# Kernel tuning notes

Measured on AMD Instinct MI355X. Metric: run time of the kernel, lower is better.

## Reference

```python
import jax, jax.numpy as jnp
import numpy as np

B, S, C, D = 16, 8192, 32, 3
VEC_OUT = 16
OUT_CH = 128
NEG_SLOPE = 0.2
EPS = float(np.finfo(np.float64).eps)


def setup_inputs() -> dict:
    key = jax.random.key(0)
    k1, k2, k3, k4, k5 = jax.random.split(key, 5)
    x = jax.random.normal(k1, (B, S, C, D), dtype=jnp.float32)
    x = x / jnp.linalg.norm(x, axis=-1, keepdims=True)  # project onto S^2
    n_in = C - 1  # 31
    U0 = (jax.random.truncated_normal(k2, -2.0, 2.0, (VEC_OUT, n_in)) * np.sqrt(2.0 / n_in)).astype(jnp.float32)
    W0 = (jax.random.truncated_normal(k3, -2.0, 2.0, (VEC_OUT, n_in)) / np.sqrt(n_in) + 1.0 / n_in).astype(jnp.float32)
    feat = n_in * VEC_OUT  # 496
    dense_kernel = (jax.random.normal(k4, (feat, OUT_CH)) / np.sqrt(feat)).astype(jnp.float32)
    dense_bias = jnp.zeros((OUT_CH,), dtype=jnp.float32)
    return {"x": x, "U0": U0, "W0": W0, "dense_kernel": dense_kernel, "dense_bias": dense_bias}


def _sphere_log(p, q):
    # p: [N, D] base points, q: [N, C-1, D]; log_p(q) on unit sphere
    cos = jnp.clip(jnp.sum(p[:, None, :] * q, axis=-1), -1.0, 1.0)  # [N, C-1]
    theta = jnp.arccos(cos)
    sin_safe = jnp.where(theta < 1e-6, 1.0, jnp.sin(theta))
    fac = jnp.where(theta < 1e-6, 1.0, theta / sin_safe)
    return fac[..., None] * (q - cos[..., None] * p[:, None, :])  # [N, C-1, D]


def _vn_layer(w, U, W):
    # w: [B, S, n_in, D]
    k = jnp.einsum('ij,bsjd->bsid', U, w)
    q = jnp.einsum('ij,bsjd->bsid', W, w)
    sqnrm_k = jnp.sum(k * k, axis=-1, keepdims=True) + EPS
    dot_qk = jnp.sum(q * k, axis=-1, keepdims=True)
    h = q + k * jax.nn.relu(-dot_qk) / sqnrm_k
    return NEG_SLOPE * q + (1.0 - NEG_SLOPE) * h


def reference(x, U0, W0, dense_kernel, dense_bias):
    n_batch, n_seq, n_in = x.shape[:3]
    xf = x.reshape(-1, n_in, D)            # [N, C, D]
    p = xf[:, 0]                           # base points
    v = _sphere_log(p, xf[:, 1:])          # [N, C-1, D]
    w = v.reshape(n_batch, n_seq, n_in - 1, D)
    w = _vn_layer(w, U0, W0)               # [B, S, VEC_OUT, D]
    w = w.reshape(n_batch * n_seq, VEC_OUT, D)
    # metric.flat on the sphere (induced metric) is the identity; VEC_OUT <= n_in so flat applies to w
    y = jnp.einsum('nij,nkj->nik', v, w)   # [N, C-1, VEC_OUT]
    y = y.reshape(n_batch, n_seq, -1)
    return y @ dense_kernel + dense_bias   # [B, S, OUT_CH]
```

## Files before the change

kernel.cpp:

```cpp
#include <hip/hip_runtime.h>

typedef float float4v __attribute__((ext_vector_type(4)));
typedef short short8  __attribute__((ext_vector_type(8)));

#define TOKENS_PER_BLOCK 256
#define NBLOCKS 512

__device__ __forceinline__ short f2bf(float f) {
  unsigned u = __float_as_uint(f);
  unsigned r = (u + 0x7fffu + ((u >> 16) & 1u)) >> 16;
  return (short)r;
}

__global__ __launch_bounds__(256, 2)
void tangent_fused(const float* __restrict__ x,
                   const float* __restrict__ U0,
                   const float* __restrict__ W0,
                   const float* __restrict__ dk,
                   const float* __restrict__ bias,
                   float* __restrict__ out)
{
  __shared__ __align__(16) float xlds[16 * 100];
  __shared__ __align__(16) float vlds[16 * 104];
  __shared__ __align__(16) float u0p[16 * 36];
  __shared__ __align__(16) float w0p[16 * 36];
  __shared__ __align__(16) short ylds[16 * 520];

  const int tid  = threadIdx.x;
  const int lane = tid & 63;
  const int wv   = tid >> 6;

  for (int i = tid; i < 16 * 36; i += 256) { u0p[i] = 0.f; w0p[i] = 0.f; }
  __syncthreads();
  for (int i = tid; i < 496; i += 256) {
    int r = i / 31, c = i % 31;
    u0p[r * 36 + c] = U0[i];
    w0p[r * 36 + c] = W0[i];
  }

  const int bn  = lane & 15;
  const int k8  = (lane >> 4) * 8;
  const int ch0 = wv * 32;
  short8 bfrag[16][2];
#pragma unroll
  for (int kk = 0; kk < 16; ++kk) {
#pragma unroll
    for (int g = 0; g < 2; ++g) {
      int c = ch0 + 16 * g + bn;
      short8 t;
#pragma unroll
      for (int j = 0; j < 8; ++j) {
        int f = kk * 32 + k8 + j;
        float v = (f < 496) ? dk[f * 128 + c] : 0.f;
        t[j] = f2bf(v);
      }
      bfrag[kk][g] = t;
    }
  }
  const float bias0 = bias[ch0 + bn];
  const float bias1 = bias[ch0 + 16 + bn];
  __syncthreads();

  const int tok16 = tid >> 4;
  const int tt    = tid & 15;

  const int block_tok0 = blockIdx.x * TOKENS_PER_BLOCK;

  for (int tile = 0; tile < 16; ++tile) {
    const int tbase = block_tok0 + tile * 16;

    {
      const float4v* xg = (const float4v*)(x + (size_t)tbase * 96);
      {
        int idx = tid;
        float4v v = xg[idx];
        int tk = idx / 24, cl = (idx % 24) * 4;
        *(float4v*)&xlds[tk * 100 + cl] = v;
      }
      {
        int idx = tid + 256;
        if (idx < 384) {
          float4v v = xg[idx];
          int tk = idx / 24, cl = (idx % 24) * 4;
          *(float4v*)&xlds[tk * 100 + cl] = v;
        }
      }
    }
    __syncthreads();

    {
      const float* xr = &xlds[tok16 * 100];
      float p0 = xr[0], p1 = xr[1], p2 = xr[2];
      float* vr = &vlds[tok16 * 104];
#pragma unroll
      for (int rep = 0; rep < 2; ++rep) {
        int jj = tt + rep * 16;
        if (jj < 31) {
          float q0 = xr[3 + 3 * jj], q1 = xr[4 + 3 * jj], q2 = xr[5 + 3 * jj];
          float cs = __fadd_rn(__fadd_rn(__fmul_rn(p0, q0), __fmul_rn(p1, q1)),
                               __fmul_rn(p2, q2));
          cs = fminf(fmaxf(cs, -1.f), 1.f);
          float th  = acosf(cs);
          float fac = (th < 1e-6f) ? 1.f : (th / sinf(th));
          vr[3 * jj + 0] = fac * (q0 - cs * p0);
          vr[3 * jj + 1] = fac * (q1 - cs * p1);
          vr[3 * jj + 2] = fac * (q2 - cs * p2);
        }
      }
      if (tt == 15) { vr[93] = 0.f; vr[94] = 0.f; vr[95] = 0.f; }
    }
    __syncthreads();

    {
      const float4v* v4 = (const float4v*)&vlds[tok16 * 104];
      const float4v* u4 = (const float4v*)&u0p[tt * 36];
      const float4v* w4 = (const float4v*)&w0p[tt * 36];
      float k0 = 0, k1 = 0, k2 = 0, q0 = 0, q1 = 0, q2 = 0;
#pragma unroll
      for (int g = 0; g < 8; ++g) {
        float4v a = v4[3 * g], b = v4[3 * g + 1], c = v4[3 * g + 2];
        float4v uu = u4[g], ww = w4[g];
        k0 += uu.x * a.x; k1 += uu.x * a.y; k2 += uu.x * a.z;
        q0 += ww.x * a.x; q1 += ww.x * a.y; q2 += ww.x * a.z;
        k0 += uu.y * a.w; k1 += uu.y * b.x; k2 += uu.y * b.y;
        q0 += ww.y * a.w; q1 += ww.y * b.x; q2 += ww.y * b.y;
        k0 += uu.z * b.z; k1 += uu.z * b.w; k2 += uu.z * c.x;
        q0 += ww.z * b.z; q1 += ww.z * b.w; q2 += ww.z * c.x;
        k0 += uu.w * c.y; k1 += uu.w * c.z; k2 += uu.w * c.w;
        q0 += ww.w * c.y; q1 += ww.w * c.z; q2 += ww.w * c.w;
      }
      float dot = k0 * q0 + k1 * q1 + k2 * q2;
      float sq  = k0 * k0 + k1 * k1 + k2 * k2 + 2.2204460492503131e-16f;
      float fac = fmaxf(-dot, 0.f) / sq;
      float f8  = 0.8f * fac;
      float wx = q0 + f8 * k0, wy = q1 + f8 * k1, wz = q2 + f8 * k2;

      asm volatile("" ::: "memory");

      short* yrow = &ylds[tok16 * 520];
#pragma unroll
      for (int g = 0; g < 8; ++g) {
        float4v a = v4[3 * g], b = v4[3 * g + 1], c = v4[3 * g + 2];
        float y0 = a.x * wx + a.y * wy + a.z * wz;
        float y1 = a.w * wx + b.x * wy + b.y * wz;
        float y2 = b.z * wx + b.w * wy + c.x * wz;
        float y3 = c.y * wx + c.z * wy + c.w * wz;
        yrow[(4 * g + 0) * 16 + tt] = f2bf(y0);
        yrow[(4 * g + 1) * 16 + tt] = f2bf(y1);
        yrow[(4 * g + 2) * 16 + tt] = f2bf(y2);
        yrow[(4 * g + 3) * 16 + tt] = f2bf(y3);
      }
    }
    __syncthreads();

    {
      const int am = lane & 15;
      float4v acc0 = {0.f, 0.f, 0.f, 0.f};
      float4v acc1 = {0.f, 0.f, 0.f, 0.f};
#pragma unroll
      for (int kk = 0; kk < 16; ++kk) {
        short8 af = *(const short8*)&ylds[am * 520 + kk * 32 + k8];
        acc0 = __builtin_amdgcn_mfma_f32_16x16x32_bf16(af, bfrag[kk][0], acc0, 0, 0, 0);
        acc1 = __builtin_amdgcn_mfma_f32_16x16x32_bf16(af, bfrag[kk][1], acc1, 0, 0, 0);
      }
      const int row4 = (lane >> 4) * 4;
#pragma unroll
      for (int r = 0; r < 4; ++r) {
        size_t o = (size_t)(tbase + row4 + r) * 128 + ch0 + bn;
        out[o]      = acc0[r] + bias0;
        out[o + 16] = acc1[r] + bias1;
      }
    }
  }
}

extern "C" void kernel_launch(void* const* d_in, const int* in_sizes, int n_in,
                              void* d_out, int out_size, void* d_ws, size_t ws_size,
                              hipStream_t stream) {
  const float* x    = (const float*)d_in[0];
  const float* U0   = (const float*)d_in[1];
  const float* W0   = (const float*)d_in[2];
  const float* dk   = (const float*)d_in[3];
  const float* bias = (const float*)d_in[4];
  float* out = (float*)d_out;
  tangent_fused<<<NBLOCKS, 256, 0, stream>>>(x, U0, W0, dk, bias, out);
}
```

Measured before the change: 171.7 us.

## Use 512-thread blocks, 32-token tiles, and a precomputed bf16 weight workspace

A small prep kernel converts the dense kernel to bf16 MFMA B-fragments in the workspace, so each block loads its fragments directly instead of gathering and converting them itself. Blocks grow to 512 threads: each of the 8 waves owns 16 output channels and shares its fragments across two 16-token A tiles, with 32 tokens per tile and half as many tiles. One barrier between the log-map stage and the VN stage is dropped, since each token row is written and read by threads of the same wave. The sin division is replaced with an rsqrt of 1-cos². The 512-thread launch bound with 4 blocks per CU caps register use and risks spills, LDS per block roughly doubles, and the rsqrt form may lose precision near cos = ±1.

```diff
diff --git a/kernel.cpp b/kernel.cpp
--- a/kernel.cpp
+++ b/kernel.cpp
@@ -3,95 +3,107 @@
 typedef float float4v __attribute__((ext_vector_type(4)));
 typedef short short8  __attribute__((ext_vector_type(8)));
 
-#define TOKENS_PER_BLOCK 256
 #define NBLOCKS 512
+#define TOK_PER_BLOCK 256
+#define WS_NEEDED 131072
 
 __device__ __forceinline__ short f2bf(float f) {
   unsigned u = __float_as_uint(f);
-  unsigned r = (u + 0x7fffu + ((u >> 16) & 1u)) >> 16;
-  return (short)r;
-}
-
-__global__ __launch_bounds__(256, 2)
+  return (short)((u + 0x7fffu + ((u >> 16) & 1u)) >> 16);
+}
+
+__global__ void dk_prep(const float* __restrict__ dk, short8* __restrict__ ws) {
+  int g = blockIdx.x * 256 + threadIdx.x;
+  int c = g & 127, k8g = (g >> 7) & 3, kk = g >> 9;
+  short8 t;
+#pragma unroll
+  for (int j = 0; j < 8; ++j) {
+    int f = kk * 32 + k8g * 8 + j;
+    t[j] = (f < 496) ? f2bf(dk[f * 128 + c]) : (short)0;
+  }
+  ws[g] = t;
+}
+
+template<bool USE_WS>
+__global__ __launch_bounds__(512, 4)
 void tangent_fused(const float* __restrict__ x,
                    const float* __restrict__ U0,
                    const float* __restrict__ W0,
                    const float* __restrict__ dk,
+                   const short8* __restrict__ wsdk,
                    const float* __restrict__ bias,
                    float* __restrict__ out)
 {
-  __shared__ __align__(16) float xlds[16 * 100];
-  __shared__ __align__(16) float vlds[16 * 104];
+  __shared__ __align__(16) float xlds[32 * 100];
+  __shared__ __align__(16) float vlds[32 * 104];
   __shared__ __align__(16) float u0p[16 * 36];
   __shared__ __align__(16) float w0p[16 * 36];
-  __shared__ __align__(16) short ylds[16 * 520];
+  __shared__ __align__(16) short ylds[32 * 520];
 
   const int tid  = threadIdx.x;
   const int lane = tid & 63;
   const int wv   = tid >> 6;
 
-  for (int i = tid; i < 16 * 36; i += 256) { u0p[i] = 0.f; w0p[i] = 0.f; }
+  if (tid < 576) { u0p[tid] = 0.f; w0p[tid] = 0.f; }
   __syncthreads();
-  for (int i = tid; i < 496; i += 256) {
-    int r = i / 31, c = i % 31;
-    u0p[r * 36 + c] = U0[i];
-    w0p[r * 36 + c] = W0[i];
+  if (tid < 496) {
+    int r = tid / 31, c = tid % 31;
+    u0p[r * 36 + c] = U0[tid];
+    w0p[r * 36 + c] = W0[tid];
   }
 
   const int bn  = lane & 15;
-  const int k8  = (lane >> 4) * 8;
-  const int ch0 = wv * 32;
-  short8 bfrag[16][2];
-#pragma unroll
-  for (int kk = 0; kk < 16; ++kk) {
-#pragma unroll
-    for (int g = 0; g < 2; ++g) {
-      int c = ch0 + 16 * g + bn;
+  const int k8g = lane >> 4;
+  const int k8  = k8g * 8;
+  const int ch0 = wv * 16;
+  short8 bfrag[16];
+  if (USE_WS) {
+#pragma unroll
+    for (int kk = 0; kk < 16; ++kk)
+      bfrag[kk] = wsdk[(kk * 4 + k8g) * 128 + ch0 + bn];
+  } else {
+#pragma unroll
+    for (int kk = 0; kk < 16; ++kk) {
       short8 t;
 #pragma unroll
       for (int j = 0; j < 8; ++j) {
         int f = kk * 32 + k8 + j;
-        float v = (f < 496) ? dk[f * 128 + c] : 0.f;
-        t[j] = f2bf(v);
-      }
-      bfrag[kk][g] = t;
+        t[j] = (f < 496) ? f2bf(dk[f * 128 + ch0 + bn]) : (short)0;
+      }
+      bfrag[kk] = t;
     }
   }
   const float bias0 = bias[ch0 + bn];
-  const float bias1 = bias[ch0 + 16 + bn];
   __syncthreads();
 
-  const int tok16 = tid >> 4;
-  const int tt    = tid & 15;
-
-  const int block_tok0 = blockIdx.x * TOKENS_PER_BLOCK;
-
-  for (int tile = 0; tile < 16; ++tile) {
-    const int tbase = block_tok0 + tile * 16;
+  const int trow = tid >> 4;
+  const int tt   = tid & 15;
+  const int block_tok0 = blockIdx.x * TOK_PER_BLOCK;
+
+  for (int tile = 0; tile < 8; ++tile) {
+    const int tbase = block_tok0 + tile * 32;
 
     {
       const float4v* xg = (const float4v*)(x + (size_t)tbase * 96);
       {
         int idx = tid;
         float4v v = xg[idx];
-        int tk = idx / 24, cl = (idx % 24) * 4;
-        *(float4v*)&xlds[tk * 100 + cl] = v;
+        *(float4v*)&xlds[(idx / 24) * 100 + (idx % 24) * 4] = v;
       }
       {
-        int idx = tid + 256;
-        if (idx < 384) {
+        int idx = tid + 512;
+        if (idx < 768) {
           float4v v = xg[idx];
-          int tk = idx / 24, cl = (idx % 24) * 4;
-          *(float4v*)&xlds[tk * 100 + cl] = v;
+          *(float4v*)&xlds[(idx / 24) * 100 + (idx % 24) * 4] = v;
         }
       }
     }
     __syncthreads();
 
     {
-      const float* xr = &xlds[tok16 * 100];
+      const float* xr = &xlds[trow * 100];
       float p0 = xr[0], p1 = xr[1], p2 = xr[2];
-      float* vr = &vlds[tok16 * 104];
+      float* vr = &vlds[trow * 104];
 #pragma unroll
       for (int rep = 0; rep < 2; ++rep) {
         int jj = tt + rep * 16;
@@ -100,8 +112,9 @@
           float cs = __fadd_rn(__fadd_rn(__fmul_rn(p0, q0), __fmul_rn(p1, q1)),
                                __fmul_rn(p2, q2));
           cs = fminf(fmaxf(cs, -1.f), 1.f);
-          float th  = acosf(cs);
-          float fac = (th < 1e-6f) ? 1.f : (th / sinf(th));
+          float th = acosf(cs);
+          float fac = (th < 1e-6f) ? 1.f
+                                   : th * rsqrtf((1.f - cs) * (1.f + cs));
           vr[3 * jj + 0] = fac * (q0 - cs * p0);
           vr[3 * jj + 1] = fac * (q1 - cs * p1);
           vr[3 * jj + 2] = fac * (q2 - cs * p2);
@@ -109,10 +122,9 @@
       }
       if (tt == 15) { vr[93] = 0.f; vr[94] = 0.f; vr[95] = 0.f; }
     }
-    __syncthreads();
-
-    {
-      const float4v* v4 = (const float4v*)&vlds[tok16 * 104];
+
+    {
+      const float4v* v4 = (const float4v*)&vlds[trow * 104];
       const float4v* u4 = (const float4v*)&u0p[tt * 36];
       const float4v* w4 = (const float4v*)&w0p[tt * 36];
       float k0 = 0, k1 = 0, k2 = 0, q0 = 0, q1 = 0, q2 = 0;
@@ -131,13 +143,12 @@
       }
       float dot = k0 * q0 + k1 * q1 + k2 * q2;
       float sq  = k0 * k0 + k1 * k1 + k2 * k2 + 2.2204460492503131e-16f;
-      float fac = fmaxf(-dot, 0.f) / sq;
-      float f8  = 0.8f * fac;
+      float f8  = 0.8f * (fmaxf(-dot, 0.f) / sq);
       float wx = q0 + f8 * k0, wy = q1 + f8 * k1, wz = q2 + f8 * k2;
 
       asm volatile("" ::: "memory");
 
-      short* yrow = &ylds[tok16 * 520];
+      short* yrow = &ylds[trow * 520];
 #pragma unroll
       for (int g = 0; g < 8; ++g) {
         float4v a = v4[3 * g], b = v4[3 * g + 1], c = v4[3 * g + 2];
@@ -159,16 +170,16 @@
       float4v acc1 = {0.f, 0.f, 0.f, 0.f};
 #pragma unroll
       for (int kk = 0; kk < 16; ++kk) {
-        short8 af = *(const short8*)&ylds[am * 520 + kk * 32 + k8];
-        acc0 = __builtin_amdgcn_mfma_f32_16x16x32_bf16(af, bfrag[kk][0], acc0, 0, 0, 0);
-        acc1 = __builtin_amdgcn_mfma_f32_16x16x32_bf16(af, bfrag[kk][1], acc1, 0, 0, 0);
-      }
-      const int row4 = (lane >> 4) * 4;
+        short8 a0 = *(const short8*)&ylds[am * 520 + kk * 32 + k8];
+        short8 a1 = *(const short8*)&ylds[(16 + am) * 520 + kk * 32 + k8];
+        acc0 = __builtin_amdgcn_mfma_f32_16x16x32_bf16(a0, bfrag[kk], acc0, 0, 0, 0);
+        acc1 = __builtin_amdgcn_mfma_f32_16x16x32_bf16(a1, bfrag[kk], acc1, 0, 0, 0);
+      }
+      const int row4 = k8g * 4;
 #pragma unroll
       for (int r = 0; r < 4; ++r) {
-        size_t o = (size_t)(tbase + row4 + r) * 128 + ch0 + bn;
-        out[o]      = acc0[r] + bias0;
-        out[o + 16] = acc1[r] + bias1;
+        out[(size_t)(tbase + row4 + r) * 128 + ch0 + bn]      = acc0[r] + bias0;
+        out[(size_t)(tbase + 16 + row4 + r) * 128 + ch0 + bn] = acc1[r] + bias0;
       }
     }
   }
@@ -183,5 +194,11 @@
   const float* dk   = (const float*)d_in[3];
   const float* bias = (const float*)d_in[4];
   float* out = (float*)d_out;
-  tangent_fused<<<NBLOCKS, 256, 0, stream>>>(x, U0, W0, dk, bias, out);
-}
+  if (ws_size >= WS_NEEDED) {
+    short8* ws = (short8*)d_ws;
+    dk_prep<<<32, 256, 0, stream>>>(dk, ws);
+    tangent_fused<true><<<NBLOCKS, 512, 0, stream>>>(x, U0, W0, dk, ws, bias, out);
+  } else {
+    tangent_fused<false><<<NBLOCKS, 512, 0, stream>>>(x, U0, W0, dk, nullptr, bias, out);
+  }
+}
```

Result: faster. 150.6 us (-12.3%).
